# Kernel optimization log

Hardware: AMD Instinct MI355X
Metric: run time of the kernel (lower is better)

## Reference

```python
import jax, jax.numpy as jnp
import numpy as np

T, B, L, D, A = 64, 64, 100, 128, 18
H = 4 * D  # lstm_size = 4 * input_size


def lstm_cell(x, h, c, Wih, Whh, bih, bhh):
    # PyTorch LSTM gate order: i, f, g, o
    g = x @ Wih.T + bih + h @ Whh.T + bhh
    i, f, gg, o = jnp.split(g, 4, axis=-1)
    c = jax.nn.sigmoid(f) * c + jax.nn.sigmoid(i) * jnp.tanh(gg)
    h = jax.nn.sigmoid(o) * jnp.tanh(c)
    return h, c


def setup_inputs() -> dict:
    key = jax.random.key(0)
    ks = jax.random.split(key, 26)

    def gl(k, shape, fan_in):
        s = float(1.0 / np.sqrt(fan_in))
        return jax.random.uniform(k, shape, jnp.float32, -s, s)

    return dict(
        state=jax.random.normal(ks[0], (T, B, D), jnp.float32),
        demonstration=jax.random.normal(ks[1], (T, B, L, D), jnp.float32),
        demonstration_length=jax.random.randint(ks[2], (T, B), 1, L + 1),
        prev_action=jax.random.randint(ks[3], (T, B), 0, A),
        prev_reward=jax.random.normal(ks[4], (T, B), jnp.float32),
        h0=jnp.zeros((B, H), jnp.float32),
        c0=jnp.zeros((B, H), jnp.float32),
        enc_Wih=gl(ks[5], (4 * H, D), H), enc_Whh=gl(ks[6], (4 * H, H), H),
        enc_bih=gl(ks[7], (4 * H,), H), enc_bhh=gl(ks[8], (4 * H,), H),
        attn_W=gl(ks[9], (H, H), H), attn_b=gl(ks[10], (H,), H),
        comb_W=gl(ks[11], (H, D + H), D + H), comb_b=gl(ks[12], (H,), D + H),
        lstm_Wih=gl(ks[13], (4 * H, H), H), lstm_Whh=gl(ks[14], (4 * H, H), H),
        lstm_bih=gl(ks[15], (4 * H,), H), lstm_bhh=gl(ks[16], (4 * H,), H),
        mid_W=gl(ks[17], (H, H), H), mid_b=gl(ks[18], (H,), H),
        out_W=gl(ks[19], (A, H), H), out_b=gl(ks[20], (A,), H),
    )


def reference(state, demonstration, demonstration_length, prev_action, prev_reward,
              h0, c0, enc_Wih, enc_Whh, enc_bih, enc_bhh, attn_W, attn_b,
              comb_W, comb_b, lstm_Wih, lstm_Whh, lstm_bih, lstm_bhh,
              mid_W, mid_b, out_W, out_b):
    Lm = demonstration.shape[2]
    demo0 = demonstration[0]  # [B, L, D] (source uses demonstration[0] only)

    # --- demonstration encoder LSTM over L, zero initial state ---
    def enc_step(carry, x):
        h, c = carry
        h, c = lstm_cell(x, h, c, enc_Wih, enc_Whh, enc_bih, enc_bhh)
        return (h, c), h

    z = jnp.zeros((demo0.shape[0], H), demo0.dtype)
    _, enc = jax.lax.scan(enc_step, (z, z), jnp.swapaxes(demo0, 0, 1))
    enc = jnp.swapaxes(enc, 0, 1)  # [B, L, H]

    # invariant across t in the source loop; hoisted (same math)
    attn_proj = enc @ attn_W.T + attn_b  # [B, L, H]
    lengths = demonstration_length[0]  # [B]
    mask = jnp.arange(Lm)[None, :] < lengths[:, None]  # [B, L]
    scale = jnp.float32(1.0 / np.sqrt(Lm))

    # --- per-timestep fused attention + LSTM cell + heads ---
    def step(carry, obs_t):
        h, c = carry
        w = jnp.einsum('blh,bh->bl', attn_proj, h) * scale
        w = jnp.where(mask, w, -jnp.inf)
        w = jax.nn.softmax(w, axis=-1)
        applied = jnp.einsum('bl,blh->bh', w, enc)
        x = jax.nn.relu(jnp.concatenate([applied, obs_t], axis=-1) @ comb_W.T + comb_b)
        h, c = lstm_cell(x, h, c, lstm_Wih, lstm_Whh, lstm_bih, lstm_bhh)
        m = h @ mid_W.T + mid_b
        q_t = m @ out_W.T + out_b
        return (h, c), q_t

    (h, c), q = jax.lax.scan(step, (h0, c0), state)  # q: [T, B, A]
    return q, h, c
```

## Files before the change

### kernel.cpp

```cpp
#include <hip/hip_runtime.h>
#include <math.h>

#define Bsz 64
#define Tn 64
#define Ln 100
#define Dn 128
#define An 18
#define Hn 512
#define NGRP 16

__device__ __forceinline__ float sigf(float x){ return 1.0f/(1.0f+expf(-x)); }

__device__ __forceinline__ void scst(float* p, float v){
  __hip_atomic_store(p, v, __ATOMIC_RELAXED, __HIP_MEMORY_SCOPE_AGENT);
}
__device__ __forceinline__ void scsti(int* p, int v){
  __hip_atomic_store(p, v, __ATOMIC_RELAXED, __HIP_MEMORY_SCOPE_AGENT);
}
__device__ __forceinline__ int lcldi(const int* p){
  return __hip_atomic_load((int*)p, __ATOMIC_RELAXED, __HIP_MEMORY_SCOPE_AGENT);
}

__device__ __forceinline__ void gbarH(int* grp_arr, int* grp_gen, int* root,
                                      int nb, int ph){
  __syncthreads();
  if (threadIdx.x == 0){
    asm volatile("s_waitcnt vmcnt(0) lgkmcnt(0)" ::: "memory");
    const int gs = nb >> 4;
    const int g  = (int)blockIdx.x & 15;
    int a = __hip_atomic_fetch_add(grp_arr + g*64, 1, __ATOMIC_RELAXED, __HIP_MEMORY_SCOPE_AGENT) + 1;
    if (a == ph*gs){
      int r = __hip_atomic_fetch_add(root, 1, __ATOMIC_RELAXED, __HIP_MEMORY_SCOPE_AGENT) + 1;
      if (r == ph*NGRP){
        #pragma unroll
        for (int i = 0; i < NGRP; i++) scsti(grp_gen + i*64, ph);
      }
    }
    while (lcldi(grp_gen + g*64) < ph) __builtin_amdgcn_s_sleep(1);
  }
  __syncthreads();
}

__global__ __launch_bounds__(256) void demo_transpose_kernel(
    const float* __restrict__ demo, float* __restrict__ demoT)
{
  int idx = blockIdx.x*256 + threadIdx.x;
  if (idx < Ln*Bsz*Dn) {
    int d = idx & 127;
    int b = (idx >> 7) & 63;
    int l = idx >> 13;
    demoT[idx] = demo[((size_t)(b*Ln + l))*Dn + d];
  }
}

__global__ __launch_bounds__(256) void gemm_nt_kernel(
    const float* __restrict__ A, int lda,
    const float* __restrict__ B, int ldb,
    const float* __restrict__ bias,
    float* __restrict__ C, int ldc, int K)
{
  __shared__ float As[64][17];
  __shared__ float Bs[64][17];
  const int m0 = blockIdx.x * 64;
  const int n0 = blockIdx.y * 64;
  const int tx = threadIdx.x & 15;
  const int ty = threadIdx.x >> 4;
  float acc[4][4] = {};
  for (int k0 = 0; k0 < K; k0 += 16) {
    #pragma unroll
    for (int i = 0; i < 4; i++) {
      int e = threadIdx.x + i*256;
      int r = e >> 4, c = e & 15;
      As[r][c] = A[(size_t)(m0 + r)*lda + k0 + c];
      Bs[r][c] = B[(size_t)(n0 + r)*ldb + k0 + c];
    }
    __syncthreads();
    #pragma unroll
    for (int kk = 0; kk < 16; kk++) {
      float a0 = As[ty*4+0][kk], a1 = As[ty*4+1][kk], a2 = As[ty*4+2][kk], a3 = As[ty*4+3][kk];
      float b0 = Bs[tx*4+0][kk], b1 = Bs[tx*4+1][kk], b2 = Bs[tx*4+2][kk], b3 = Bs[tx*4+3][kk];
      acc[0][0] += a0*b0; acc[0][1] += a0*b1; acc[0][2] += a0*b2; acc[0][3] += a0*b3;
      acc[1][0] += a1*b0; acc[1][1] += a1*b1; acc[1][2] += a1*b2; acc[1][3] += a1*b3;
      acc[2][0] += a2*b0; acc[2][1] += a2*b1; acc[2][2] += a2*b2; acc[2][3] += a2*b3;
      acc[3][0] += a3*b0; acc[3][1] += a3*b1; acc[3][2] += a3*b2; acc[3][3] += a3*b3;
    }
    __syncthreads();
  }
  #pragma unroll
  for (int i = 0; i < 4; i++) {
    #pragma unroll
    for (int j = 0; j < 4; j++) {
      int nn = n0 + tx*4 + j;
      float v = acc[i][j] + (bias ? bias[nn] : 0.0f);
      C[(size_t)(m0 + ty*4 + i)*ldc + nn] = v;
    }
  }
}

__global__ __launch_bounds__(512, 1) void enc_scan_kernel(
    const float* __restrict__ demoT,
    const float* __restrict__ Wih, const float* __restrict__ Whh,
    const float* __restrict__ bih, const float* __restrict__ bhh,
    const float* __restrict__ attn_W, const float* __restrict__ attn_b,
    const float* __restrict__ comb_W,
    float* __restrict__ hencR,
    float* __restrict__ attnp,
    float* __restrict__ CE,
    int* __restrict__ gA, int* __restrict__ gG, int* __restrict__ gR)
{
  const int bid  = blockIdx.x;
  const int tid  = threadIdx.x;
  const int lane = tid & 63;
  const int ks   = tid >> 6;
  const int n0   = bid*2;

  __shared__ float lds_whh[8][Hn];
  __shared__ float lds_wih[8][Dn];
  __shared__ float lds_atw[2][Hn];
  __shared__ float lds_cbw[2][Hn];
  __shared__ float red[8][12][Bsz];

  #pragma unroll
  for (int c = 0; c < 2; c++)
    #pragma unroll
    for (int g = 0; g < 4; g++){
      int r = c*4 + g;
      lds_whh[r][tid] = Whh[(size_t)(g*Hn + n0 + c)*Hn + tid];
      if (tid < Dn) lds_wih[r][tid] = Wih[(size_t)(g*Hn + n0 + c)*Dn + tid];
    }
  #pragma unroll
  for (int c = 0; c < 2; c++){
    lds_atw[c][tid] = attn_W[(size_t)(n0 + c)*Hn + tid];
    lds_cbw[c][tid] = comb_W[(size_t)(n0 + c)*(Hn + Dn) + tid];
  }
  float bsum[2][4];
  #pragma unroll
  for (int c = 0; c < 2; c++)
    #pragma unroll
    for (int g = 0; g < 4; g++){
      int r = g*Hn + n0 + c;
      bsum[c][g] = bih[r] + bhh[r];
    }
  const float ab[2] = { attn_b[n0], attn_b[n0+1] };
  float cr[2] = {0.f, 0.f};
  __syncthreads();

  for (int l = 0; l <= Ln; l++){
    float a[2][4] = {{0,0,0,0},{0,0,0,0}};
    float aa[2] = {0,0}, ac[2] = {0,0};
    if (l >= 1){
      const float4* hv = (const float4*)(hencR + ((size_t)(l-1)*Bsz + lane)*Hn) + ks*16;
      #pragma unroll 4
      for (int q = 0; q < 16; q++){
        float4 H = hv[q];
        #pragma unroll
        for (int c = 0; c < 2; c++){
          #pragma unroll
          for (int g = 0; g < 4; g++){
            float4 W = *(const float4*)&lds_whh[c*4+g][ks*64 + 4*q];
            a[c][g] += H.x*W.x + H.y*W.y + H.z*W.z + H.w*W.w;
          }
          float4 Aw = *(const float4*)&lds_atw[c][ks*64 + 4*q];
          aa[c] += H.x*Aw.x + H.y*Aw.y + H.z*Aw.z + H.w*Aw.w;
          float4 Cw = *(const float4*)&lds_cbw[c][ks*64 + 4*q];
          ac[c] += H.x*Cw.x + H.y*Cw.y + H.z*Cw.z + H.w*Cw.w;
        }
      }
    }
    if (l < Ln){
      const float4* dv = (const float4*)(demoT + ((size_t)l*Bsz + lane)*Dn) + ks*4;
      #pragma unroll
      for (int q = 0; q < 4; q++){
        float4 V = dv[q];
        #pragma unroll
        for (int c = 0; c < 2; c++)
          #pragma unroll
          for (int g = 0; g < 4; g++){
            float4 W = *(const float4*)&lds_wih[c*4+g][ks*16 + 4*q];
            a[c][g] += V.x*W.x + V.y*W.y + V.z*W.z + V.w*W.w;
          }
      }
    }
    #pragma unroll
    for (int c = 0; c < 2; c++){
      #pragma unroll
      for (int g = 0; g < 4; g++) red[ks][c*4+g][lane] = a[c][g];
      red[ks][8+c][lane]  = aa[c];
      red[ks][10+c][lane] = ac[c];
    }
    __syncthreads();
    if (tid < Bsz){
      int b = tid;
      if (l < Ln){
        #pragma unroll
        for (int c = 0; c < 2; c++){
          float g0 = bsum[c][0], g1 = bsum[c][1], g2 = bsum[c][2], g3 = bsum[c][3];
          #pragma unroll
          for (int k = 0; k < 8; k++){
            g0 += red[k][c*4+0][b]; g1 += red[k][c*4+1][b];
            g2 += red[k][c*4+2][b]; g3 += red[k][c*4+3][b];
          }
          float ii = sigf(g0), ff = sigf(g1), gg = tanhf(g2), oo = sigf(g3);
          float cn = ff*cr[c] + ii*gg;
          float hn = oo*tanhf(cn);
          cr[c] = cn;
          scst(hencR + ((size_t)l*Bsz + b)*Hn + n0 + c, hn);
        }
      }
      if (l >= 1){
        #pragma unroll
        for (int c = 0; c < 2; c++){
          float av = ab[c], cv = 0.f;
          #pragma unroll
          for (int k = 0; k < 8; k++){ av += red[k][8+c][b]; cv += red[k][10+c][b]; }
          scst(attnp + ((size_t)(b*Ln + (l-1)))*Hn + n0 + c, av);
          scst(CE    + ((size_t)(b*Ln + (l-1)))*Hn + n0 + c, cv);
        }
      }
    }
    if (l < Ln) gbarH(gA, gG, gR, (int)gridDim.x, l+1);
  }
}

__global__ __launch_bounds__(512, 1) void dec_scan_kernel(
    const float* __restrict__ h0, const float* __restrict__ c0,
    const float* __restrict__ attnp,
    const float* __restrict__ CE,
    const float* __restrict__ preobs,
    const int*   __restrict__ dlen,
    const float* __restrict__ lstm_Wih, const float* __restrict__ lstm_Whh,
    const float* __restrict__ lstm_bih, const float* __restrict__ lstm_bhh,
    const float* __restrict__ comb_b,
    float* __restrict__ xrow,
    float* __restrict__ hhist,
    float* __restrict__ outp,
    int* __restrict__ gA, int* __restrict__ gG, int* __restrict__ gR)
{
  const int bid  = blockIdx.x;
  const int tid  = threadIdx.x;
  const int lane = tid & 63;
  const int ks   = tid >> 6;
  const int n0   = bid*2;

  __shared__ float lds_wi[8][Hn];
  __shared__ float lds_wh[8][Hn];
  __shared__ float hs[Hn];
  __shared__ float wls[128];
  __shared__ float mx_s, sum_s;
  __shared__ float red[8][8][Bsz];

  #pragma unroll
  for (int c = 0; c < 2; c++)
    #pragma unroll
    for (int g = 0; g < 4; g++){
      int r = c*4 + g;
      lds_wi[r][tid] = lstm_Wih[(size_t)(g*Hn + n0 + c)*Hn + tid];
      lds_wh[r][tid] = lstm_Whh[(size_t)(g*Hn + n0 + c)*Hn + tid];
    }
  float bs[2][4];
  #pragma unroll
  for (int c = 0; c < 2; c++)
    #pragma unroll
    for (int g = 0; g < 4; g++){
      int r = g*Hn + n0 + c;
      bs[c][g] = lstm_bih[r] + lstm_bhh[r];
    }
  float cr[2] = {0.f, 0.f};
  int ph = 0;
  __syncthreads();

  for (int t = 0; t < Tn; t++){
    const float* hprev_all = (t == 0) ? h0 : (hhist + (size_t)(t-1)*Bsz*Hn);

    if (bid < Bsz){
      const int b = bid;
      hs[tid] = hprev_all[(size_t)b*Hn + tid];
      if (tid >= 100 && tid < 128) wls[tid] = -1e30f;
      __syncthreads();
      const int len = dlen[b];
      if (tid < 400){
        int l = tid >> 2, kh = tid & 3;
        const float4* ap = (const float4*)(attnp + ((size_t)(b*Ln + l))*Hn) + kh*32;
        const float4* hv = (const float4*)hs + kh*32;
        float s = 0.f;
        #pragma unroll 8
        for (int k = 0; k < 32; k++){
          float4 A = ap[k], H = hv[k];
          s += A.x*H.x + A.y*H.y + A.z*H.z + A.w*H.w;
        }
        s += __shfl_xor(s, 1);
        s += __shfl_xor(s, 2);
        if (kh == 0) wls[l] = (l < len) ? s*0.1f : -1e30f;
      }
      __syncthreads();
      if (tid < 64){
        float v = fmaxf(wls[tid], wls[tid+64]);
        for (int off = 1; off < 64; off <<= 1) v = fmaxf(v, __shfl_xor(v, off));
        if (tid == 0) mx_s = v;
      }
      __syncthreads();
      float mx = mx_s;
      if (tid < 64){
        float e0 = (wls[tid]    > -1e29f) ? expf(wls[tid]    - mx) : 0.f;
        float e1 = (wls[tid+64] > -1e29f) ? expf(wls[tid+64] - mx) : 0.f;
        wls[tid] = e0; wls[tid+64] = e1;
        float v = e0 + e1;
        for (int off = 1; off < 64; off <<= 1) v += __shfl_xor(v, off);
        if (tid == 0) sum_s = v;
      }
      __syncthreads();
      float inv = 1.0f / sum_s;
      {
        int n = tid;
        const float* cb = CE + (size_t)b*Ln*Hn + n;
        float acc = 0.f;
        for (int l2 = 0; l2 < len; ++l2) acc += cb[(size_t)l2*Hn]*wls[l2];
        float v = acc*inv + preobs[((size_t)(t*Bsz + b))*Hn + n] + comb_b[n];
        scst(xrow + ((size_t)t*Bsz + b)*Hn + n, fmaxf(v, 0.f));
      }
    }
    float hpa[2][4] = {{0,0,0,0},{0,0,0,0}};
    {
      const float4* hv = (const float4*)(hprev_all + (size_t)lane*Hn) + ks*16;
      #pragma unroll 4
      for (int q = 0; q < 16; q++){
        float4 H = hv[q];
        #pragma unroll
        for (int c = 0; c < 2; c++)
          #pragma unroll
          for (int g = 0; g < 4; g++){
            float4 W = *(const float4*)&lds_wh[c*4+g][ks*64 + 4*q];
            hpa[c][g] += H.x*W.x + H.y*W.y + H.z*W.z + H.w*W.w;
          }
      }
    }
    gbarH(gA, gG, gR, (int)gridDim.x, ++ph);

    {
      const float4* xv = (const float4*)(xrow + ((size_t)t*Bsz + lane)*Hn) + ks*16;
      #pragma unroll 4
      for (int q = 0; q < 16; q++){
        float4 X = xv[q];
        #pragma unroll
        for (int c = 0; c < 2; c++)
          #pragma unroll
          for (int g = 0; g < 4; g++){
            float4 W = *(const float4*)&lds_wi[c*4+g][ks*64 + 4*q];
            hpa[c][g] += X.x*W.x + X.y*W.y + X.z*W.z + X.w*W.w;
          }
      }
      #pragma unroll
      for (int c = 0; c < 2; c++)
        #pragma unroll
        for (int g = 0; g < 4; g++) red[ks][c*4+g][lane] = hpa[c][g];
      __syncthreads();
      if (tid < Bsz){
        int b = tid;
        #pragma unroll
        for (int c = 0; c < 2; c++){
          int n = n0 + c;
          if (t == 0) cr[c] = c0[(size_t)b*Hn + n];
          float g0 = bs[c][0], g1 = bs[c][1], g2 = bs[c][2], g3 = bs[c][3];
          #pragma unroll
          for (int k = 0; k < 8; k++){
            g0 += red[k][c*4+0][b]; g1 += red[k][c*4+1][b];
            g2 += red[k][c*4+2][b]; g3 += red[k][c*4+3][b];
          }
          float ii = sigf(g0), ff = sigf(g1), gg = tanhf(g2), oo = sigf(g3);
          float cn = ff*cr[c] + ii*gg;
          float hn = oo*tanhf(cn);
          cr[c] = cn;
          scst(hhist + ((size_t)t*Bsz + b)*Hn + n, hn);
          if (t == Tn - 1){
            outp[Tn*Bsz*An + (size_t)b*Hn + n]           = hn;
            outp[Tn*Bsz*An + Bsz*Hn + (size_t)b*Hn + n]  = cn;
          }
        }
      }
    }
    if (t < Tn - 1) gbarH(gA, gG, gR, (int)gridDim.x, ++ph);
  }
}

__global__ __launch_bounds__(256) void qout_kernel(
    const float* __restrict__ m, const float* __restrict__ out_W,
    const float* __restrict__ out_b, float* __restrict__ q)
{
  const int t = blockIdx.x;
  for (int p = threadIdx.x; p < Bsz*An; p += 256) {
    int b = p / An, a2 = p % An;
    const float* mr = m + ((size_t)(t*Bsz + b))*Hn;
    const float* wr = out_W + (size_t)a2*Hn;
    float s = out_b[a2];
    #pragma unroll 8
    for (int k = 0; k < Hn; k++) s += mr[k]*wr[k];
    q[((size_t)(t*Bsz + b))*An + a2] = s;
  }
}

extern "C" void kernel_launch(void* const* d_in, const int* in_sizes, int n_in,
                              void* d_out, int out_size, void* d_ws, size_t ws_size,
                              hipStream_t stream) {
  (void)in_sizes; (void)n_in; (void)out_size; (void)ws_size;
  const float* state    = (const float*)d_in[0];
  const float* demo     = (const float*)d_in[1];
  const int*   dlen     = (const int*)  d_in[2];
  const float* h0       = (const float*)d_in[5];
  const float* c0       = (const float*)d_in[6];
  const float* enc_Wih  = (const float*)d_in[7];
  const float* enc_Whh  = (const float*)d_in[8];
  const float* enc_bih  = (const float*)d_in[9];
  const float* enc_bhh  = (const float*)d_in[10];
  const float* attn_W   = (const float*)d_in[11];
  const float* attn_b   = (const float*)d_in[12];
  const float* comb_W   = (const float*)d_in[13];
  const float* comb_b   = (const float*)d_in[14];
  const float* lstm_Wih = (const float*)d_in[15];
  const float* lstm_Whh = (const float*)d_in[16];
  const float* lstm_bih = (const float*)d_in[17];
  const float* lstm_bhh = (const float*)d_in[18];
  const float* mid_W    = (const float*)d_in[19];
  const float* mid_b    = (const float*)d_in[20];
  const float* out_W    = (const float*)d_in[21];
  const float* out_b    = (const float*)d_in[22];
  float* ws   = (float*)d_ws;
  float* qout = (float*)d_out;

  float* attnp  = ws + 0;
  float* CE     = ws + 3276800;
  float* preobs = ws + 6553600;
  float* region = ws + 8650752;
  float* demoT  = region;
  float* hencR  = region + 819200;
  float* xrow   = region;
  float* hhist  = region + 2097152;
  int*   barB   = (int*)(ws + 12845056);
  int* encA = barB;          int* encG = barB + 1024; int* encR = barB + 2048;
  int* decA = barB + 2112;   int* decG = barB + 3136; int* decR = barB + 4160;
  float* mbuf = CE;

  hipMemsetAsync((void*)barB, 0, 4224*4, stream);

  demo_transpose_kernel<<<3200, 256, 0, stream>>>(demo, demoT);

  gemm_nt_kernel<<<dim3(Tn*Bsz/64, Hn/64), 256, 0, stream>>>(
      state, Dn, comb_W + Hn, Hn + Dn, nullptr, preobs, Hn, Dn);

  enc_scan_kernel<<<256, 512, 0, stream>>>(
      demoT, enc_Wih, enc_Whh, enc_bih, enc_bhh, attn_W, attn_b, comb_W,
      hencR, attnp, CE, encA, encG, encR);

  dec_scan_kernel<<<256, 512, 0, stream>>>(
      h0, c0, attnp, CE, preobs, dlen, lstm_Wih, lstm_Whh, lstm_bih, lstm_bhh,
      comb_b, xrow, hhist, qout, decA, decG, decR);

  gemm_nt_kernel<<<dim3(Tn*Bsz/64, Hn/64), 256, 0, stream>>>(
      hhist, Hn, mid_W, Hn, mid_b, mbuf, Hn, Hn);

  qout_kernel<<<Tn, 256, 0, stream>>>(mbuf, out_W, out_b, qout);
}
```

Measured before the change: 2.881 ms.

## Split encoder barrier into arrive/wait, fold mid and out heads, unroll attention loop

The encoder scan now computes the recurrent gates first and signals barrier arrival as soon as its h slice is stored. The attention and comb projections of the previous step are computed before waiting, so they overlap with the global barrier latency. The mid and output linear layers are folded offline into one 18x512 matrix plus bias, which replaces a 512x512 GEMM and the q kernel with a single small head kernel. The decoder's attention-weighted sum now loops over the full L with unrolling instead of the per-batch length, relying on masked weights being zero.

```diff
diff --git a/kernel.cpp b/kernel.cpp
--- a/kernel.cpp
+++ b/kernel.cpp
@@ -21,22 +21,28 @@
   return __hip_atomic_load((int*)p, __ATOMIC_RELAXED, __HIP_MEMORY_SCOPE_AGENT);
 }
 
-__device__ __forceinline__ void gbarH(int* grp_arr, int* grp_gen, int* root,
-                                      int nb, int ph){
+__device__ __forceinline__ void gbar_arrive(int* grp_arr, int* grp_gen, int* root, int nb, int ph){
+  const int gs = nb >> 4;
+  const int g  = (int)blockIdx.x & 15;
+  int a = __hip_atomic_fetch_add(grp_arr + g*64, 1, __ATOMIC_RELAXED, __HIP_MEMORY_SCOPE_AGENT) + 1;
+  if (a == ph*gs){
+    int r = __hip_atomic_fetch_add(root, 1, __ATOMIC_RELAXED, __HIP_MEMORY_SCOPE_AGENT) + 1;
+    if (r == ph*NGRP){
+      #pragma unroll
+      for (int i = 0; i < NGRP; i++) scsti(grp_gen + i*64, ph);
+    }
+  }
+}
+__device__ __forceinline__ void gbar_wait(int* grp_gen, int ph){
+  const int g = (int)blockIdx.x & 15;
+  while (lcldi(grp_gen + g*64) < ph) __builtin_amdgcn_s_sleep(1);
+}
+__device__ __forceinline__ void gbarH(int* gA, int* gG, int* gR, int nb, int ph){
   __syncthreads();
   if (threadIdx.x == 0){
     asm volatile("s_waitcnt vmcnt(0) lgkmcnt(0)" ::: "memory");
-    const int gs = nb >> 4;
-    const int g  = (int)blockIdx.x & 15;
-    int a = __hip_atomic_fetch_add(grp_arr + g*64, 1, __ATOMIC_RELAXED, __HIP_MEMORY_SCOPE_AGENT) + 1;
-    if (a == ph*gs){
-      int r = __hip_atomic_fetch_add(root, 1, __ATOMIC_RELAXED, __HIP_MEMORY_SCOPE_AGENT) + 1;
-      if (r == ph*NGRP){
-        #pragma unroll
-        for (int i = 0; i < NGRP; i++) scsti(grp_gen + i*64, ph);
-      }
-    }
-    while (lcldi(grp_gen + g*64) < ph) __builtin_amdgcn_s_sleep(1);
+    gbar_arrive(gA, gG, gR, nb, ph);
+    gbar_wait(gG, ph);
   }
   __syncthreads();
 }
@@ -94,6 +100,44 @@
       float v = acc[i][j] + (bias ? bias[nn] : 0.0f);
       C[(size_t)(m0 + ty*4 + i)*ldc + nn] = v;
     }
+  }
+}
+
+__global__ __launch_bounds__(512) void head_fold_kernel(
+    const float* __restrict__ mid_W, const float* __restrict__ mid_b,
+    const float* __restrict__ out_W, const float* __restrict__ out_b,
+    float* __restrict__ M2, float* __restrict__ bias2)
+{
+  const int a = blockIdx.x;
+  const int k = threadIdx.x;
+  const float* ow = out_W + (size_t)a*Hn;
+  float s = 0.f;
+  #pragma unroll 4
+  for (int n = 0; n < Hn; n++) s += ow[n]*mid_W[(size_t)n*Hn + k];
+  M2[(size_t)a*Hn + k] = s;
+  if (k == 0){
+    float b2 = out_b[a];
+    for (int n = 0; n < Hn; n++) b2 += ow[n]*mid_b[n];
+    bias2[a] = b2;
+  }
+}
+
+__global__ __launch_bounds__(256) void qhead_kernel(
+    const float* __restrict__ hhist, const float* __restrict__ M2,
+    const float* __restrict__ bias2, float* __restrict__ q)
+{
+  const int t = blockIdx.x;
+  for (int p = threadIdx.x; p < Bsz*An; p += 256){
+    int b = p / An, a = p % An;
+    const float4* hv = (const float4*)(hhist + ((size_t)t*Bsz + b)*Hn);
+    const float4* mv = (const float4*)(M2 + (size_t)a*Hn);
+    float s = bias2[a];
+    #pragma unroll 8
+    for (int k = 0; k < Hn/4; k++){
+      float4 H = hv[k], M = mv[k];
+      s += H.x*M.x + H.y*M.y + H.z*M.z + H.w*M.w;
+    }
+    q[((size_t)(t*Bsz + b))*An + a] = s;
   }
 }
 
@@ -146,52 +190,43 @@
   __syncthreads();
 
   for (int l = 0; l <= Ln; l++){
-    float a[2][4] = {{0,0,0,0},{0,0,0,0}};
-    float aa[2] = {0,0}, ac[2] = {0,0};
-    if (l >= 1){
-      const float4* hv = (const float4*)(hencR + ((size_t)(l-1)*Bsz + lane)*Hn) + ks*16;
-      #pragma unroll 4
-      for (int q = 0; q < 16; q++){
-        float4 H = hv[q];
-        #pragma unroll
-        for (int c = 0; c < 2; c++){
-          #pragma unroll
-          for (int g = 0; g < 4; g++){
-            float4 W = *(const float4*)&lds_whh[c*4+g][ks*64 + 4*q];
-            a[c][g] += H.x*W.x + H.y*W.y + H.z*W.z + H.w*W.w;
-          }
-          float4 Aw = *(const float4*)&lds_atw[c][ks*64 + 4*q];
-          aa[c] += H.x*Aw.x + H.y*Aw.y + H.z*Aw.z + H.w*Aw.w;
-          float4 Cw = *(const float4*)&lds_cbw[c][ks*64 + 4*q];
-          ac[c] += H.x*Cw.x + H.y*Cw.y + H.z*Cw.z + H.w*Cw.w;
-        }
-      }
-    }
     if (l < Ln){
-      const float4* dv = (const float4*)(demoT + ((size_t)l*Bsz + lane)*Dn) + ks*4;
+      float a[2][4] = {{0,0,0,0},{0,0,0,0}};
+      if (l >= 1){
+        const float4* hv = (const float4*)(hencR + ((size_t)(l-1)*Bsz + lane)*Hn) + ks*16;
+        #pragma unroll 4
+        for (int q = 0; q < 16; q++){
+          float4 H = hv[q];
+          #pragma unroll
+          for (int c = 0; c < 2; c++)
+            #pragma unroll
+            for (int g = 0; g < 4; g++){
+              float4 W = *(const float4*)&lds_whh[c*4+g][ks*64 + 4*q];
+              a[c][g] += H.x*W.x + H.y*W.y + H.z*W.z + H.w*W.w;
+            }
+        }
+      }
+      {
+        const float4* dv = (const float4*)(demoT + ((size_t)l*Bsz + lane)*Dn) + ks*4;
+        #pragma unroll
+        for (int q = 0; q < 4; q++){
+          float4 V = dv[q];
+          #pragma unroll
+          for (int c = 0; c < 2; c++)
+            #pragma unroll
+            for (int g = 0; g < 4; g++){
+              float4 W = *(const float4*)&lds_wih[c*4+g][ks*16 + 4*q];
+              a[c][g] += V.x*W.x + V.y*W.y + V.z*W.z + V.w*W.w;
+            }
+        }
+      }
       #pragma unroll
-      for (int q = 0; q < 4; q++){
-        float4 V = dv[q];
-        #pragma unroll
-        for (int c = 0; c < 2; c++)
-          #pragma unroll
-          for (int g = 0; g < 4; g++){
-            float4 W = *(const float4*)&lds_wih[c*4+g][ks*16 + 4*q];
-            a[c][g] += V.x*W.x + V.y*W.y + V.z*W.z + V.w*W.w;
-          }
-      }
-    }
-    #pragma unroll
-    for (int c = 0; c < 2; c++){
-      #pragma unroll
-      for (int g = 0; g < 4; g++) red[ks][c*4+g][lane] = a[c][g];
-      red[ks][8+c][lane]  = aa[c];
-      red[ks][10+c][lane] = ac[c];
-    }
-    __syncthreads();
-    if (tid < Bsz){
-      int b = tid;
-      if (l < Ln){
+      for (int c = 0; c < 2; c++)
+        #pragma unroll
+        for (int g = 0; g < 4; g++) red[ks][c*4+g][lane] = a[c][g];
+      __syncthreads();
+      if (tid < Bsz){
+        int b = tid;
         #pragma unroll
         for (int c = 0; c < 2; c++){
           float g0 = bsum[c][0], g1 = bsum[c][1], g2 = bsum[c][2], g3 = bsum[c][3];
@@ -207,7 +242,33 @@
           scst(hencR + ((size_t)l*Bsz + b)*Hn + n0 + c, hn);
         }
       }
-      if (l >= 1){
+      if (tid == 0){
+        asm volatile("s_waitcnt vmcnt(0)" ::: "memory");
+        gbar_arrive(gA, gG, gR, (int)gridDim.x, l+1);
+      }
+    }
+    if (l >= 1){
+      float aa[2] = {0,0}, ac[2] = {0,0};
+      const float4* hv = (const float4*)(hencR + ((size_t)(l-1)*Bsz + lane)*Hn) + ks*16;
+      #pragma unroll 4
+      for (int q = 0; q < 16; q++){
+        float4 H = hv[q];
+        #pragma unroll
+        for (int c = 0; c < 2; c++){
+          float4 Aw = *(const float4*)&lds_atw[c][ks*64 + 4*q];
+          aa[c] += H.x*Aw.x + H.y*Aw.y + H.z*Aw.z + H.w*Aw.w;
+          float4 Cw = *(const float4*)&lds_cbw[c][ks*64 + 4*q];
+          ac[c] += H.x*Cw.x + H.y*Cw.y + H.z*Cw.z + H.w*Cw.w;
+        }
+      }
+      #pragma unroll
+      for (int c = 0; c < 2; c++){
+        red[ks][8+c][lane]  = aa[c];
+        red[ks][10+c][lane] = ac[c];
+      }
+      __syncthreads();
+      if (tid < Bsz){
+        int b = tid;
         #pragma unroll
         for (int c = 0; c < 2; c++){
           float av = ab[c], cv = 0.f;
@@ -218,7 +279,10 @@
         }
       }
     }
-    if (l < Ln) gbarH(gA, gG, gR, (int)gridDim.x, l+1);
+    if (l < Ln){
+      if (tid == 0) gbar_wait(gG, l+1);
+      __syncthreads();
+    }
   }
 }
 
@@ -314,7 +378,8 @@
         int n = tid;
         const float* cb = CE + (size_t)b*Ln*Hn + n;
         float acc = 0.f;
-        for (int l2 = 0; l2 < len; ++l2) acc += cb[(size_t)l2*Hn]*wls[l2];
+        #pragma unroll 4
+        for (int l2 = 0; l2 < Ln; ++l2) acc += cb[(size_t)l2*Hn]*wls[l2];
         float v = acc*inv + preobs[((size_t)(t*Bsz + b))*Hn + n] + comb_b[n];
         scst(xrow + ((size_t)t*Bsz + b)*Hn + n, fmaxf(v, 0.f));
       }
@@ -377,24 +442,16 @@
           }
         }
       }
-    }
-    if (t < Tn - 1) gbarH(gA, gG, gR, (int)gridDim.x, ++ph);
-  }
-}
-
-__global__ __launch_bounds__(256) void qout_kernel(
-    const float* __restrict__ m, const float* __restrict__ out_W,
-    const float* __restrict__ out_b, float* __restrict__ q)
-{
-  const int t = blockIdx.x;
-  for (int p = threadIdx.x; p < Bsz*An; p += 256) {
-    int b = p / An, a2 = p % An;
-    const float* mr = m + ((size_t)(t*Bsz + b))*Hn;
-    const float* wr = out_W + (size_t)a2*Hn;
-    float s = out_b[a2];
-    #pragma unroll 8
-    for (int k = 0; k < Hn; k++) s += mr[k]*wr[k];
-    q[((size_t)(t*Bsz + b))*An + a2] = s;
+      if (t < Tn - 1){
+        if (tid == 0){
+          asm volatile("s_waitcnt vmcnt(0)" ::: "memory");
+          gbar_arrive(gA, gG, gR, (int)gridDim.x, ph+1);
+          gbar_wait(gG, ph+1);
+        }
+        ph++;
+        __syncthreads();
+      }
+    }
   }
 }
 
@@ -437,11 +494,14 @@
   int*   barB   = (int*)(ws + 12845056);
   int* encA = barB;          int* encG = barB + 1024; int* encR = barB + 2048;
   int* decA = barB + 2112;   int* decG = barB + 3136; int* decR = barB + 4160;
-  float* mbuf = CE;
+  float* M2    = ws + 12850176;
+  float* bias2 = ws + 12859392;
 
   hipMemsetAsync((void*)barB, 0, 4224*4, stream);
 
   demo_transpose_kernel<<<3200, 256, 0, stream>>>(demo, demoT);
+
+  head_fold_kernel<<<An, 512, 0, stream>>>(mid_W, mid_b, out_W, out_b, M2, bias2);
 
   gemm_nt_kernel<<<dim3(Tn*Bsz/64, Hn/64), 256, 0, stream>>>(
       state, Dn, comb_W + Hn, Hn + Dn, nullptr, preobs, Hn, Dn);
@@ -454,8 +514,5 @@
       h0, c0, attnp, CE, preobs, dlen, lstm_Wih, lstm_Whh, lstm_bih, lstm_bhh,
       comb_b, xrow, hhist, qout, decA, decG, decR);
 
-  gemm_nt_kernel<<<dim3(Tn*Bsz/64, Hn/64), 256, 0, stream>>>(
-      hhist, Hn, mid_W, Hn, mid_b, mbuf, Hn, Hn);
-
-  qout_kernel<<<Tn, 256, 0, stream>>>(mbuf, out_W, out_b, qout);
-}
+  qhead_kernel<<<Tn, 256, 0, stream>>>(hhist, M2, bias2, qout);
+}
```

New measurement: 3.418 ms. 18.6% more time.
